# Optimization experiments

Hardware: AMD Instinct MI355X
Metric: run time of the kernel (lower is better)

The kernel has to match this reference:

```python
import jax, jax.numpy as jnp
import numpy as np

NEG_SLOPE = 0.2  # leakyrelu negative_slope from init

def _lrelu(x):
    return jax.nn.leaky_relu(x, NEG_SLOPE)

def setup_inputs() -> dict:
    key = jax.random.key(0)
    k1, k2, k3 = jax.random.split(key, 3)
    B, N, Fin, Fout = 8, 2048, 128, 64
    x = jax.random.normal(k1, (B, N, Fin), dtype=jnp.float32)
    W = jax.random.normal(k2, (Fin, Fout), dtype=jnp.float32) * (1.414 / np.sqrt(Fin))
    a = jax.random.normal(k3, (2 * Fout, 1), dtype=jnp.float32) * 0.1
    return {"x": x, "W": W, "a": a}

def reference(x, W, a):
    # x: (B, N, Fin), W: (Fin, Fout), a: (2*Fout, 1)
    Fout = W.shape[1]
    h = jnp.matmul(x, W)  # (B, N, Fout)
    a1 = a[:Fout, 0]      # attends to source node i
    a2 = a[Fout:, 0]      # attends to target node j
    # e[b,i,j] = leakyrelu(h[b,i]@a1 + h[b,j]@a2); avoids O(N^2*2F) repeat+cat
    s1 = jnp.einsum('bnf,f->bn', h, a1)  # (B, N)
    s2 = jnp.einsum('bnf,f->bn', h, a2)  # (B, N)
    e = _lrelu(s1[:, :, None] + s2[:, None, :])  # (B, N, N)
    attention = jax.nn.softmax(e, axis=1)  # softmax over dim=1, as in source
    # dropout in eval mode: identity
    h_prime = jnp.matmul(attention, h)  # (B, N, Fout)
    return _lrelu(h_prime)
```

## Files before the change

### kernel.cpp

```cpp
#include <hip/hip_runtime.h>
#include <math.h>

#define B 8
#define N 2048
#define NP1 2049
#define K 2048
#define KP1 2049
#define FIN 128
#define FOUT 64
#define NS 0.2f
#define NCH 64
#define CHS 32

__device__ __forceinline__ int bucketOf(float v) {
  int q = (int)floorf((v + 8.0f) * 128.0f);
  return min(max(q, 0), K - 1);
}

__device__ __forceinline__ int wscan_add_i(int v, int lane) {
#pragma unroll
  for (int off = 1; off < 64; off <<= 1) {
    int o = __shfl_up(v, off, 64);
    v += (lane >= off) ? o : 0;
  }
  return v;
}
__device__ __forceinline__ float wscan_add_f(float v, int lane) {
#pragma unroll
  for (int off = 1; off < 64; off <<= 1) {
    float o = __shfl_up(v, off, 64);
    v += (lane >= off) ? o : 0.f;
  }
  return v;
}

#define RPB 32
__global__ __launch_bounds__(256, 2) void k_hs(
    const float* __restrict__ x, const float* __restrict__ W,
    const float* __restrict__ a, float* __restrict__ h,
    float* __restrict__ s1, float* __restrict__ s2,
    float* __restrict__ u, float* __restrict__ uq,
    float* __restrict__ e2, float* __restrict__ eq2) {
  __shared__ float xs[RPB * FIN];
  const int row0 = blockIdx.x * RPB;
  const int lane = threadIdx.x & 63;
  const int wv = threadIdx.x >> 6;

  {
    const float4* src = (const float4*)(x + (size_t)row0 * FIN);
    float4* dst = (float4*)xs;
#pragma unroll
    for (int t = 0; t < 4; ++t)
      dst[threadIdx.x + 256 * t] = src[threadIdx.x + 256 * t];
  }

  float w[FIN];
#pragma unroll
  for (int k = 0; k < FIN; ++k) w[k] = W[k * FOUT + lane];
  const float a1 = a[lane];
  const float a2 = a[FOUT + lane];
  __syncthreads();

  for (int n = 0; n < 8; ++n) {
    const int r = wv * 8 + n;
    const float* xr = xs + r * FIN;
    float ac0 = 0.f, ac1 = 0.f, ac2 = 0.f, ac3 = 0.f;
#pragma unroll
    for (int k4 = 0; k4 < FIN; k4 += 4) {
      float4 xv = *(const float4*)(xr + k4);
      ac0 = fmaf(xv.x, w[k4 + 0], ac0);
      ac1 = fmaf(xv.y, w[k4 + 1], ac1);
      ac2 = fmaf(xv.z, w[k4 + 2], ac2);
      ac3 = fmaf(xv.w, w[k4 + 3], ac3);
    }
    const float acc = (ac0 + ac1) + (ac2 + ac3);
    const int row = row0 + r;
    h[(size_t)row * FOUT + lane] = acc;

    float v1 = acc * a1;
    float v2 = acc * a2;
#pragma unroll
    for (int off = 32; off > 0; off >>= 1) {
      v1 += __shfl_xor(v1, off, 64);
      v2 += __shfl_xor(v2, off, 64);
    }
    if (lane == 0) {
      s1[row] = v1;
      s2[row] = v2;
      u[row] = expf(v1);
      uq[row] = expf(NS * v1);
      e2[row] = expf(v2);
      eq2[row] = expf(NS * v2);
    }
  }
}

__global__ __launch_bounds__(1024) void k_bucket(
    const float* __restrict__ s1, const float* __restrict__ s2,
    const float* __restrict__ u, const float* __restrict__ uq,
    int* __restrict__ start1, float* __restrict__ elemS1,
    float* __restrict__ elemU, float* __restrict__ elemUq,
    float* __restrict__ slotPrefU, float* __restrict__ slotPrefQ,
    int* __restrict__ start2, float* __restrict__ elemS2,
    int* __restrict__ idx2) {
  __shared__ int cnt[K];
  __shared__ int cur[K];
  __shared__ float eS[N], eU[N], eQ[N];
  __shared__ int eJ[N];
  __shared__ int wt[16];
  __shared__ float wtU[16], wtQ[16];

  const int type = blockIdx.x & 1;
  const int b = blockIdx.x >> 1;
  const int tid = threadIdx.x;
  const int lane = tid & 63;
  const int wv = tid >> 6;
  const float* key = (type ? s2 : s1) + b * N;

  cnt[tid] = 0; cnt[tid + 1024] = 0;
  __syncthreads();
  const float k0 = key[tid], k1 = key[tid + 1024];
  const int q0 = bucketOf(k0), q1 = bucketOf(k1);
  atomicAdd(&cnt[q0], 1);
  atomicAdd(&cnt[q1], 1);
  __syncthreads();

  const int c0 = cnt[2 * tid], c1 = cnt[2 * tid + 1];
  const int loc = c0 + c1;
  const int incl = wscan_add_i(loc, lane);
  if (lane == 63) wt[wv] = incl;
  __syncthreads();
  int cross = 0;
#pragma unroll
  for (int w2 = 0; w2 < 16; ++w2) cross += (w2 < wv) ? wt[w2] : 0;
  const int ex = cross + incl - loc;
  cnt[2 * tid] = ex;       cnt[2 * tid + 1] = ex + c0;
  cur[2 * tid] = ex;       cur[2 * tid + 1] = ex + c0;
  __syncthreads();

  {
    int slot = atomicAdd(&cur[q0], 1);
    if (type == 0) { eS[slot] = k0; eU[slot] = u[b * N + tid]; eQ[slot] = uq[b * N + tid]; }
    else           { eS[slot] = k0; eJ[slot] = tid; }
    slot = atomicAdd(&cur[q1], 1);
    if (type == 0) { eS[slot] = k1; eU[slot] = u[b * N + tid + 1024]; eQ[slot] = uq[b * N + tid + 1024]; }
    else           { eS[slot] = k1; eJ[slot] = tid + 1024; }
  }
  __syncthreads();

  if (type == 1) {
    elemS2[b * N + tid] = eS[tid];  elemS2[b * N + tid + 1024] = eS[tid + 1024];
    idx2[b * N + tid] = eJ[tid];    idx2[b * N + tid + 1024] = eJ[tid + 1024];
    start2[b * KP1 + tid] = cnt[tid];  start2[b * KP1 + tid + 1024] = cnt[tid + 1024];
    if (tid == 0) start2[b * KP1 + K] = N;
    return;
  }
  elemS1[b * N + tid] = eS[tid];  elemS1[b * N + tid + 1024] = eS[tid + 1024];
  elemU[b * N + tid] = eU[tid];   elemU[b * N + tid + 1024] = eU[tid + 1024];
  elemUq[b * N + tid] = eQ[tid];  elemUq[b * N + tid + 1024] = eQ[tid + 1024];
  start1[b * KP1 + tid] = cnt[tid];  start1[b * KP1 + tid + 1024] = cnt[tid + 1024];
  if (tid == 0) start1[b * KP1 + K] = N;

  const float u0 = eU[2 * tid], u1 = eU[2 * tid + 1];
  const float g0 = eQ[2 * tid], g1 = eQ[2 * tid + 1];
  const float locU = u0 + u1, locQ = g0 + g1;
  const float iU = wscan_add_f(locU, lane);
  const float iQ = wscan_add_f(locQ, lane);
  if (lane == 63) { wtU[wv] = iU; wtQ[wv] = iQ; }
  __syncthreads();
  float crU = 0.f, crQ = 0.f, totU = 0.f, totQ = 0.f;
#pragma unroll
  for (int w2 = 0; w2 < 16; ++w2) {
    const float au = wtU[w2], aq = wtQ[w2];
    crU += (w2 < wv) ? au : 0.f;
    crQ += (w2 < wv) ? aq : 0.f;
    totU += au; totQ += aq;
  }
  const float exU = crU + iU - locU, exQ = crQ + iQ - locQ;
  slotPrefU[b * NP1 + 2 * tid] = exU;  slotPrefU[b * NP1 + 2 * tid + 1] = exU + u0;
  slotPrefQ[b * NP1 + 2 * tid] = exQ;  slotPrefQ[b * NP1 + 2 * tid + 1] = exQ + g0;
  if (tid == 0) { slotPrefU[b * NP1 + N] = totU; slotPrefQ[b * NP1 + N] = totQ; }
}

__global__ void k_z(const float* __restrict__ elemS1, const float* __restrict__ elemU,
                    const float* __restrict__ elemUq, const float* __restrict__ slotPrefU,
                    const float* __restrict__ slotPrefQ, const int* __restrict__ start1,
                    const float* __restrict__ elemS2, const int* __restrict__ idx2,
                    const float* __restrict__ e2, const float* __restrict__ eq2,
                    float* __restrict__ Aslot, float* __restrict__ Bslot) {
  const int g = blockIdx.x * 256 + threadIdx.x;
  const int b = g >> 11;
  const int s = g & (N - 1);
  const float t = -elemS2[b * N + s];
  const int j = idx2[b * N + s];
  const int q = bucketOf(t);
  const int sb = start1[b * KP1 + q], se = start1[b * KP1 + q + 1];
  float PuC = slotPrefU[b * NP1 + sb];
  float PqC = slotPrefQ[b * NP1 + sb];
  for (int s2i = sb; s2i < se; ++s2i) {
    const bool lt = elemS1[b * N + s2i] < t;
    PuC += lt ? elemU[b * N + s2i] : 0.f;
    PqC += lt ? elemUq[b * N + s2i] : 0.f;
  }
  const float totU = slotPrefU[b * NP1 + N];
  const float SU = totU - PuC;
  const float E = e2[b * N + j], Eq = eq2[b * N + j];
  const float Z = E * SU + Eq * PqC;
  Aslot[b * N + s] = E / Z;
  Bslot[b * N + s] = Eq / Z;
}

__global__ void k_scan1(const float* __restrict__ Aslot, const float* __restrict__ Bslot,
                        const float* __restrict__ h, const int* __restrict__ idx2,
                        float* __restrict__ ctA, float* __restrict__ ctB) {
  const int b = blockIdx.x >> 4;
  const int chunk = (blockIdx.x & 15) * 4 + (threadIdx.x >> 6);
  const int f = threadIdx.x & 63;
  float ta = 0.f, tb = 0.f;
#pragma unroll 4
  for (int rr = 0; rr < CHS; ++rr) {
    const int r = chunk * CHS + rr;
    const int j = idx2[b * N + r];
    const float hv = h[((size_t)b * N + j) * FOUT + f];
    ta = fmaf(Aslot[b * N + r], hv, ta);
    tb = fmaf(Bslot[b * N + r], hv, tb);
  }
  ctA[(b * NCH + chunk) * FOUT + f] = ta;
  ctB[(b * NCH + chunk) * FOUT + f] = tb;
}

__global__ void k_scan2(const float* __restrict__ Aslot, const float* __restrict__ Bslot,
                        const float* __restrict__ h, const int* __restrict__ idx2,
                        const float* __restrict__ ctA, const float* __restrict__ ctB,
                        float* __restrict__ SA, float* __restrict__ PB) {
  __shared__ float cA[NCH * FOUT];
  __shared__ float cB[NCH * FOUT];
  const int b = blockIdx.x >> 4;
  const int chunk = (blockIdx.x & 15) * 4 + (threadIdx.x >> 6);
  const int f = threadIdx.x & 63;

  for (int t = threadIdx.x; t < NCH * FOUT; t += 256) {
    cA[t] = ctA[b * NCH * FOUT + t];
    cB[t] = ctB[b * NCH * FOUT + t];
  }
  __syncthreads();

  float offA = 0.f, offB = 0.f;
#pragma unroll 8
  for (int c2 = 0; c2 < NCH; ++c2) {
    const float va = cA[c2 * FOUT + f];
    const float vb = cB[c2 * FOUT + f];
    if (c2 > chunk) offA += va;
    if (c2 < chunk) offB += vb;
  }

  float run = offB;
  for (int rr = 0; rr < CHS; ++rr) {
    const int r = chunk * CHS + rr;
    const int j = idx2[b * N + r];
    const float hv = h[((size_t)b * N + j) * FOUT + f];
    run = fmaf(Bslot[b * N + r], hv, run);
    PB[((size_t)b * NP1 + r + 1) * FOUT + f] = run;
  }
  run = offA;
  for (int rr = CHS - 1; rr >= 0; --rr) {
    const int r = chunk * CHS + rr;
    const int j = idx2[b * N + r];
    const float hv = h[((size_t)b * N + j) * FOUT + f];
    run = fmaf(Aslot[b * N + r], hv, run);
    SA[((size_t)b * NP1 + r) * FOUT + f] = run;
  }
  if (chunk == 0) {
    PB[((size_t)b * NP1 + 0) * FOUT + f] = 0.f;
    SA[((size_t)b * NP1 + N) * FOUT + f] = 0.f;
  }
}

__global__ void k_out(const float* __restrict__ s1r, const float* __restrict__ u,
                      const float* __restrict__ uq, const int* __restrict__ start2,
                      const float* __restrict__ elemS2, const int* __restrict__ idx2,
                      const float* __restrict__ Aslot, const float* __restrict__ Bslot,
                      const float* __restrict__ h, const float* __restrict__ SA,
                      const float* __restrict__ PB, float* __restrict__ out) {
  const int wv = threadIdx.x >> 6;
  const int lane = threadIdx.x & 63;
  const int row = blockIdx.x * 4 + wv;
  const int b = row >> 11;
  const float t = -s1r[row];
  const int q = bucketOf(t);
  const int sb = start2[b * KP1 + q], se = start2[b * KP1 + q + 1];

  float sa = SA[((size_t)b * NP1 + se) * FOUT + lane];
  float pb = PB[((size_t)b * NP1 + sb) * FOUT + lane];
  for (int s = sb; s < se; ++s) {
    const float s2v = elemS2[b * N + s];
    const int j = idx2[b * N + s];
    const float hv = h[((size_t)b * N + j) * FOUT + lane];
    if (s2v >= t) sa = fmaf(Aslot[b * N + s], hv, sa);
    else          pb = fmaf(Bslot[b * N + s], hv, pb);
  }
  const float v = u[row] * sa + uq[row] * pb;
  out[(size_t)row * FOUT + lane] = v >= 0.f ? v : NS * v;
}

extern "C" void kernel_launch(void* const* d_in, const int* in_sizes, int n_in,
                              void* d_out, int out_size, void* d_ws, size_t ws_size,
                              hipStream_t stream) {
  const float* x = (const float*)d_in[0];
  const float* W = (const float*)d_in[1];
  const float* a = (const float*)d_in[2];
  float* out = (float*)d_out;

  float* ws = (float*)d_ws;
  float* h = ws;
  float* s1 = h + (size_t)B * N * FOUT;
  float* s2 = s1 + B * N;
  float* u = s2 + B * N;
  float* uq = u + B * N;
  float* e2 = uq + B * N;
  float* eq2 = e2 + B * N;
  float* elemS1 = eq2 + B * N;
  float* elemU = elemS1 + B * N;
  float* elemUq = elemU + B * N;
  float* elemS2 = elemUq + B * N;
  float* Aslot = elemS2 + B * N;
  float* Bslot = Aslot + B * N;
  float* slotPrefU = Bslot + B * N;
  float* slotPrefQ = slotPrefU + B * NP1;
  int* idx2 = (int*)(slotPrefQ + B * NP1);
  int* start1 = idx2 + B * N;
  int* start2 = start1 + B * KP1;
  float* ctA = (float*)(start2 + B * KP1);
  float* ctB = ctA + B * NCH * FOUT;
  float* SA = ctB + B * NCH * FOUT;
  float* PB = SA + (size_t)B * NP1 * FOUT;

  k_hs<<<B * N / RPB, 256, 0, stream>>>(x, W, a, h, s1, s2, u, uq, e2, eq2);
  k_bucket<<<2 * B, 1024, 0, stream>>>(s1, s2, u, uq, start1, elemS1, elemU, elemUq,
                                       slotPrefU, slotPrefQ, start2, elemS2, idx2);
  k_z<<<B * (N / 256), 256, 0, stream>>>(elemS1, elemU, elemUq, slotPrefU, slotPrefQ,
                                         start1, elemS2, idx2, e2, eq2, Aslot, Bslot);
  k_scan1<<<B * 16, 256, 0, stream>>>(Aslot, Bslot, h, idx2, ctA, ctB);
  k_scan2<<<B * 16, 256, 0, stream>>>(Aslot, Bslot, h, idx2, ctA, ctB, SA, PB);
  k_out<<<B * N / 4, 256, 0, stream>>>(s1, u, uq, start2, elemS2, idx2, Aslot, Bslot,
                                       h, SA, PB, out);
}
```

Measured before the change: 63.25 us.

## Halve bucket count, double scan chunks, recompute exps inline, preload scan operands

Measured after the change: 67.79 us. 7.2% more time.

```diff
diff --git a/kernel.cpp b/kernel.cpp
--- a/kernel.cpp
+++ b/kernel.cpp
@@ -4,16 +4,16 @@
 #define B 8
 #define N 2048
 #define NP1 2049
-#define K 2048
-#define KP1 2049
 #define FIN 128
 #define FOUT 64
 #define NS 0.2f
-#define NCH 64
-#define CHS 32
+#define K 1024
+#define KP1 1025
+#define NCH 128
+#define CHS 16
 
 __device__ __forceinline__ int bucketOf(float v) {
-  int q = (int)floorf((v + 8.0f) * 128.0f);
+  int q = (int)floorf((v + 8.0f) * 64.0f);
   return min(max(q, 0), K - 1);
 }
 
@@ -38,9 +38,7 @@
 __global__ __launch_bounds__(256, 2) void k_hs(
     const float* __restrict__ x, const float* __restrict__ W,
     const float* __restrict__ a, float* __restrict__ h,
-    float* __restrict__ s1, float* __restrict__ s2,
-    float* __restrict__ u, float* __restrict__ uq,
-    float* __restrict__ e2, float* __restrict__ eq2) {
+    float* __restrict__ s1, float* __restrict__ s2) {
   __shared__ float xs[RPB * FIN];
   const int row0 = blockIdx.x * RPB;
   const int lane = threadIdx.x & 63;
@@ -87,17 +85,12 @@
     if (lane == 0) {
       s1[row] = v1;
       s2[row] = v2;
-      u[row] = expf(v1);
-      uq[row] = expf(NS * v1);
-      e2[row] = expf(v2);
-      eq2[row] = expf(NS * v2);
     }
   }
 }
 
 __global__ __launch_bounds__(1024) void k_bucket(
     const float* __restrict__ s1, const float* __restrict__ s2,
-    const float* __restrict__ u, const float* __restrict__ uq,
     int* __restrict__ start1, float* __restrict__ elemS1,
     float* __restrict__ elemU, float* __restrict__ elemUq,
     float* __restrict__ slotPrefU, float* __restrict__ slotPrefQ,
@@ -105,9 +98,11 @@
     int* __restrict__ idx2) {
   __shared__ int cnt[K];
   __shared__ int cur[K];
-  __shared__ float eS[N], eU[N], eQ[N];
+  __shared__ float eS[N];
+  __shared__ float eU[N];
+  __shared__ float eQ[N];
   __shared__ int eJ[N];
-  __shared__ int wt[16];
+  __shared__ int wtI[16];
   __shared__ float wtU[16], wtQ[16];
 
   const int type = blockIdx.x & 1;
@@ -117,7 +112,7 @@
   const int wv = tid >> 6;
   const float* key = (type ? s2 : s1) + b * N;
 
-  cnt[tid] = 0; cnt[tid + 1024] = 0;
+  cnt[tid] = 0;
   __syncthreads();
   const float k0 = key[tid], k1 = key[tid + 1024];
   const int q0 = bucketOf(k0), q1 = bucketOf(k1);
@@ -125,40 +120,50 @@
   atomicAdd(&cnt[q1], 1);
   __syncthreads();
 
-  const int c0 = cnt[2 * tid], c1 = cnt[2 * tid + 1];
-  const int loc = c0 + c1;
-  const int incl = wscan_add_i(loc, lane);
-  if (lane == 63) wt[wv] = incl;
-  __syncthreads();
-  int cross = 0;
-#pragma unroll
-  for (int w2 = 0; w2 < 16; ++w2) cross += (w2 < wv) ? wt[w2] : 0;
-  const int ex = cross + incl - loc;
-  cnt[2 * tid] = ex;       cnt[2 * tid + 1] = ex + c0;
-  cur[2 * tid] = ex;       cur[2 * tid + 1] = ex + c0;
-  __syncthreads();
-
   {
-    int slot = atomicAdd(&cur[q0], 1);
-    if (type == 0) { eS[slot] = k0; eU[slot] = u[b * N + tid]; eQ[slot] = uq[b * N + tid]; }
-    else           { eS[slot] = k0; eJ[slot] = tid; }
-    slot = atomicAdd(&cur[q1], 1);
-    if (type == 0) { eS[slot] = k1; eU[slot] = u[b * N + tid + 1024]; eQ[slot] = uq[b * N + tid + 1024]; }
-    else           { eS[slot] = k1; eJ[slot] = tid + 1024; }
+    const int v = cnt[tid];
+    const int incl = wscan_add_i(v, lane);
+    if (lane == 63) wtI[wv] = incl;
+    __syncthreads();
+    int cross = 0;
+#pragma unroll
+    for (int w = 0; w < 16; ++w) cross += (w < wv) ? wtI[w] : 0;
+    const int ex = cross + incl - v;
+    cnt[tid] = ex;
+    cur[tid] = ex;
+  }
+  __syncthreads();
+
+  if (type == 0) {
+    int sl = atomicAdd(&cur[q0], 1);
+    eS[sl] = k0; eU[sl] = expf(k0); eQ[sl] = expf(NS * k0);
+    sl = atomicAdd(&cur[q1], 1);
+    eS[sl] = k1; eU[sl] = expf(k1); eQ[sl] = expf(NS * k1);
+  } else {
+    int sl = atomicAdd(&cur[q0], 1);
+    eS[sl] = k0; eJ[sl] = tid;
+    sl = atomicAdd(&cur[q1], 1);
+    eS[sl] = k1; eJ[sl] = tid + 1024;
   }
   __syncthreads();
 
   if (type == 1) {
-    elemS2[b * N + tid] = eS[tid];  elemS2[b * N + tid + 1024] = eS[tid + 1024];
-    idx2[b * N + tid] = eJ[tid];    idx2[b * N + tid + 1024] = eJ[tid + 1024];
-    start2[b * KP1 + tid] = cnt[tid];  start2[b * KP1 + tid + 1024] = cnt[tid + 1024];
+    elemS2[b * N + tid] = eS[tid];
+    elemS2[b * N + tid + 1024] = eS[tid + 1024];
+    idx2[b * N + tid] = eJ[tid];
+    idx2[b * N + tid + 1024] = eJ[tid + 1024];
+    start2[b * KP1 + tid] = cnt[tid];
     if (tid == 0) start2[b * KP1 + K] = N;
     return;
   }
-  elemS1[b * N + tid] = eS[tid];  elemS1[b * N + tid + 1024] = eS[tid + 1024];
-  elemU[b * N + tid] = eU[tid];   elemU[b * N + tid + 1024] = eU[tid + 1024];
-  elemUq[b * N + tid] = eQ[tid];  elemUq[b * N + tid + 1024] = eQ[tid + 1024];
-  start1[b * KP1 + tid] = cnt[tid];  start1[b * KP1 + tid + 1024] = cnt[tid + 1024];
+
+  elemS1[b * N + tid] = eS[tid];
+  elemS1[b * N + tid + 1024] = eS[tid + 1024];
+  elemU[b * N + tid] = eU[tid];
+  elemU[b * N + tid + 1024] = eU[tid + 1024];
+  elemUq[b * N + tid] = eQ[tid];
+  elemUq[b * N + tid + 1024] = eQ[tid + 1024];
+  start1[b * KP1 + tid] = cnt[tid];
   if (tid == 0) start1[b * KP1 + K] = N;
 
   const float u0 = eU[2 * tid], u1 = eU[2 * tid + 1];
@@ -170,42 +175,42 @@
   __syncthreads();
   float crU = 0.f, crQ = 0.f, totU = 0.f, totQ = 0.f;
 #pragma unroll
-  for (int w2 = 0; w2 < 16; ++w2) {
-    const float au = wtU[w2], aq = wtQ[w2];
-    crU += (w2 < wv) ? au : 0.f;
-    crQ += (w2 < wv) ? aq : 0.f;
+  for (int w = 0; w < 16; ++w) {
+    const float au = wtU[w], aq = wtQ[w];
+    crU += (w < wv) ? au : 0.f;
+    crQ += (w < wv) ? aq : 0.f;
     totU += au; totQ += aq;
   }
   const float exU = crU + iU - locU, exQ = crQ + iQ - locQ;
-  slotPrefU[b * NP1 + 2 * tid] = exU;  slotPrefU[b * NP1 + 2 * tid + 1] = exU + u0;
-  slotPrefQ[b * NP1 + 2 * tid] = exQ;  slotPrefQ[b * NP1 + 2 * tid + 1] = exQ + g0;
+  slotPrefU[b * NP1 + 2 * tid] = exU;
+  slotPrefU[b * NP1 + 2 * tid + 1] = exU + u0;
+  slotPrefQ[b * NP1 + 2 * tid] = exQ;
+  slotPrefQ[b * NP1 + 2 * tid + 1] = exQ + g0;
   if (tid == 0) { slotPrefU[b * NP1 + N] = totU; slotPrefQ[b * NP1 + N] = totQ; }
 }
 
 __global__ void k_z(const float* __restrict__ elemS1, const float* __restrict__ elemU,
                     const float* __restrict__ elemUq, const float* __restrict__ slotPrefU,
                     const float* __restrict__ slotPrefQ, const int* __restrict__ start1,
-                    const float* __restrict__ elemS2, const int* __restrict__ idx2,
-                    const float* __restrict__ e2, const float* __restrict__ eq2,
+                    const float* __restrict__ elemS2,
                     float* __restrict__ Aslot, float* __restrict__ Bslot) {
   const int g = blockIdx.x * 256 + threadIdx.x;
   const int b = g >> 11;
   const int s = g & (N - 1);
-  const float t = -elemS2[b * N + s];
-  const int j = idx2[b * N + s];
+  const float s2v = elemS2[b * N + s];
+  const float t = -s2v;
   const int q = bucketOf(t);
   const int sb = start1[b * KP1 + q], se = start1[b * KP1 + q + 1];
-  float PuC = slotPrefU[b * NP1 + sb];
-  float PqC = slotPrefQ[b * NP1 + sb];
-  for (int s2i = sb; s2i < se; ++s2i) {
-    const bool lt = elemS1[b * N + s2i] < t;
-    PuC += lt ? elemU[b * N + s2i] : 0.f;
-    PqC += lt ? elemUq[b * N + s2i] : 0.f;
+  float Pu = slotPrefU[b * NP1 + sb];
+  float Pq = slotPrefQ[b * NP1 + sb];
+  for (int i = sb; i < se; ++i) {
+    const bool lt = elemS1[b * N + i] < t;
+    Pu += lt ? elemU[b * N + i] : 0.f;
+    Pq += lt ? elemUq[b * N + i] : 0.f;
   }
   const float totU = slotPrefU[b * NP1 + N];
-  const float SU = totU - PuC;
-  const float E = e2[b * N + j], Eq = eq2[b * N + j];
-  const float Z = E * SU + Eq * PqC;
+  const float E = expf(s2v), Eq = expf(NS * s2v);
+  const float Z = E * (totU - Pu) + Eq * Pq;
   Aslot[b * N + s] = E / Z;
   Bslot[b * N + s] = Eq / Z;
 }
@@ -213,35 +218,55 @@
 __global__ void k_scan1(const float* __restrict__ Aslot, const float* __restrict__ Bslot,
                         const float* __restrict__ h, const int* __restrict__ idx2,
                         float* __restrict__ ctA, float* __restrict__ ctB) {
-  const int b = blockIdx.x >> 4;
-  const int chunk = (blockIdx.x & 15) * 4 + (threadIdx.x >> 6);
+  const int b = blockIdx.x >> 5;
+  const int chunk = (blockIdx.x & 31) * 4 + (threadIdx.x >> 6);
   const int f = threadIdx.x & 63;
+  const int s0 = chunk * CHS;
+
+  float hv[CHS], av[CHS], bv[CHS];
+#pragma unroll
+  for (int rr = 0; rr < CHS; ++rr) {
+    const int s = s0 + rr;
+    const int j = idx2[b * N + s];
+    hv[rr] = h[((size_t)b * N + j) * FOUT + f];
+    av[rr] = Aslot[b * N + s];
+    bv[rr] = Bslot[b * N + s];
+  }
   float ta = 0.f, tb = 0.f;
-#pragma unroll 4
+#pragma unroll
   for (int rr = 0; rr < CHS; ++rr) {
-    const int r = chunk * CHS + rr;
-    const int j = idx2[b * N + r];
-    const float hv = h[((size_t)b * N + j) * FOUT + f];
-    ta = fmaf(Aslot[b * N + r], hv, ta);
-    tb = fmaf(Bslot[b * N + r], hv, tb);
+    ta = fmaf(av[rr], hv[rr], ta);
+    tb = fmaf(bv[rr], hv[rr], tb);
   }
   ctA[(b * NCH + chunk) * FOUT + f] = ta;
   ctB[(b * NCH + chunk) * FOUT + f] = tb;
 }
 
-__global__ void k_scan2(const float* __restrict__ Aslot, const float* __restrict__ Bslot,
-                        const float* __restrict__ h, const int* __restrict__ idx2,
-                        const float* __restrict__ ctA, const float* __restrict__ ctB,
-                        float* __restrict__ SA, float* __restrict__ PB) {
+__global__ __launch_bounds__(256) void k_scan2(
+    const float* __restrict__ Aslot, const float* __restrict__ Bslot,
+    const float* __restrict__ h, const int* __restrict__ idx2,
+    const float* __restrict__ ctA, const float* __restrict__ ctB,
+    float* __restrict__ SA, float* __restrict__ PB) {
   __shared__ float cA[NCH * FOUT];
   __shared__ float cB[NCH * FOUT];
-  const int b = blockIdx.x >> 4;
-  const int chunk = (blockIdx.x & 15) * 4 + (threadIdx.x >> 6);
+  const int b = blockIdx.x >> 5;
+  const int chunk = (blockIdx.x & 31) * 4 + (threadIdx.x >> 6);
   const int f = threadIdx.x & 63;
+  const int s0 = chunk * CHS;
 
   for (int t = threadIdx.x; t < NCH * FOUT; t += 256) {
     cA[t] = ctA[b * NCH * FOUT + t];
     cB[t] = ctB[b * NCH * FOUT + t];
+  }
+
+  float hv[CHS], av[CHS], bv[CHS];
+#pragma unroll
+  for (int rr = 0; rr < CHS; ++rr) {
+    const int s = s0 + rr;
+    const int j = idx2[b * N + s];
+    hv[rr] = h[((size_t)b * N + j) * FOUT + f];
+    av[rr] = Aslot[b * N + s];
+    bv[rr] = Bslot[b * N + s];
   }
   __syncthreads();
 
@@ -255,20 +280,16 @@
   }
 
   float run = offB;
+#pragma unroll
   for (int rr = 0; rr < CHS; ++rr) {
-    const int r = chunk * CHS + rr;
-    const int j = idx2[b * N + r];
-    const float hv = h[((size_t)b * N + j) * FOUT + f];
-    run = fmaf(Bslot[b * N + r], hv, run);
-    PB[((size_t)b * NP1 + r + 1) * FOUT + f] = run;
+    run = fmaf(bv[rr], hv[rr], run);
+    PB[((size_t)b * NP1 + s0 + rr + 1) * FOUT + f] = run;
   }
   run = offA;
+#pragma unroll
   for (int rr = CHS - 1; rr >= 0; --rr) {
-    const int r = chunk * CHS + rr;
-    const int j = idx2[b * N + r];
-    const float hv = h[((size_t)b * N + j) * FOUT + f];
-    run = fmaf(Aslot[b * N + r], hv, run);
-    SA[((size_t)b * NP1 + r) * FOUT + f] = run;
+    run = fmaf(av[rr], hv[rr], run);
+    SA[((size_t)b * NP1 + s0 + rr) * FOUT + f] = run;
   }
   if (chunk == 0) {
     PB[((size_t)b * NP1 + 0) * FOUT + f] = 0.f;
@@ -276,19 +297,25 @@
   }
 }
 
-__global__ void k_out(const float* __restrict__ s1r, const float* __restrict__ u,
-                      const float* __restrict__ uq, const int* __restrict__ start2,
-                      const float* __restrict__ elemS2, const int* __restrict__ idx2,
-                      const float* __restrict__ Aslot, const float* __restrict__ Bslot,
-                      const float* __restrict__ h, const float* __restrict__ SA,
-                      const float* __restrict__ PB, float* __restrict__ out) {
+__global__ void k_out(const float* __restrict__ s1,
+                      const int* __restrict__ start2,
+                      const float* __restrict__ elemS2,
+                      const int* __restrict__ idx2,
+                      const float* __restrict__ Aslot,
+                      const float* __restrict__ Bslot,
+                      const float* __restrict__ h,
+                      const float* __restrict__ SA,
+                      const float* __restrict__ PB,
+                      float* __restrict__ out) {
   const int wv = threadIdx.x >> 6;
   const int lane = threadIdx.x & 63;
   const int row = blockIdx.x * 4 + wv;
   const int b = row >> 11;
-  const float t = -s1r[row];
+  const float s1v = s1[row];
+  const float t = -s1v;
   const int q = bucketOf(t);
-  const int sb = start2[b * KP1 + q], se = start2[b * KP1 + q + 1];
+  const int sb = start2[b * KP1 + q];
+  const int se = start2[b * KP1 + q + 1];
 
   float sa = SA[((size_t)b * NP1 + se) * FOUT + lane];
   float pb = PB[((size_t)b * NP1 + sb) * FOUT + lane];
@@ -299,7 +326,8 @@
     if (s2v >= t) sa = fmaf(Aslot[b * N + s], hv, sa);
     else          pb = fmaf(Bslot[b * N + s], hv, pb);
   }
-  const float v = u[row] * sa + uq[row] * pb;
+  const float uu = expf(s1v), uqv = expf(NS * s1v);
+  const float v = uu * sa + uqv * pb;
   out[(size_t)row * FOUT + lane] = v >= 0.f ? v : NS * v;
 }
 
@@ -315,11 +343,7 @@
   float* h = ws;
   float* s1 = h + (size_t)B * N * FOUT;
   float* s2 = s1 + B * N;
-  float* u = s2 + B * N;
-  float* uq = u + B * N;
-  float* e2 = uq + B * N;
-  float* eq2 = e2 + B * N;
-  float* elemS1 = eq2 + B * N;
+  float* elemS1 = s2 + B * N;
   float* elemU = elemS1 + B * N;
   float* elemUq = elemU + B * N;
   float* elemS2 = elemUq + B * N;
@@ -331,17 +355,17 @@
   int* start1 = idx2 + B * N;
   int* start2 = start1 + B * KP1;
   float* ctA = (float*)(start2 + B * KP1);
-  float* ctB = ctA + B * NCH * FOUT;
-  float* SA = ctB + B * NCH * FOUT;
+  float* ctB = ctA + (size_t)B * NCH * FOUT;
+  float* SA = ctB + (size_t)B * NCH * FOUT;
   float* PB = SA + (size_t)B * NP1 * FOUT;
 
-  k_hs<<<B * N / RPB, 256, 0, stream>>>(x, W, a, h, s1, s2, u, uq, e2, eq2);
-  k_bucket<<<2 * B, 1024, 0, stream>>>(s1, s2, u, uq, start1, elemS1, elemU, elemUq,
+  k_hs<<<B * N / RPB, 256, 0, stream>>>(x, W, a, h, s1, s2);
+  k_bucket<<<2 * B, 1024, 0, stream>>>(s1, s2, start1, elemS1, elemU, elemUq,
                                        slotPrefU, slotPrefQ, start2, elemS2, idx2);
-  k_z<<<B * (N / 256), 256, 0, stream>>>(elemS1, elemU, elemUq, slotPrefU, slotPrefQ,
-                                         start1, elemS2, idx2, e2, eq2, Aslot, Bslot);
-  k_scan1<<<B * 16, 256, 0, stream>>>(Aslot, Bslot, h, idx2, ctA, ctB);
-  k_scan2<<<B * 16, 256, 0, stream>>>(Aslot, Bslot, h, idx2, ctA, ctB, SA, PB);
-  k_out<<<B * N / 4, 256, 0, stream>>>(s1, u, uq, start2, elemS2, idx2, Aslot, Bslot,
+  k_z<<<B * (N / 256), 256, 0, stream>>>(elemS1, elemU, elemUq, slotPrefU,
+                                         slotPrefQ, start1, elemS2, Aslot, Bslot);
+  k_scan1<<<B * 32, 256, 0, stream>>>(Aslot, Bslot, h, idx2, ctA, ctB);
+  k_scan2<<<B * 32, 256, 0, stream>>>(Aslot, Bslot, h, idx2, ctA, ctB, SA, PB);
+  k_out<<<B * N / 4, 256, 0, stream>>>(s1, start2, elemS2, idx2, Aslot, Bslot,
                                        h, SA, PB, out);
 }
```
